# Kernel tuning notes

Hardware: AMD Instinct MI355X
Metric: run time of the kernel (lower is better)

## Reference

```python
import jax, jax.numpy as jnp
import numpy as np
from jax import lax

N = 16384
K = 16
EPS = 1e-5


def setup_inputs() -> dict:
    key = jax.random.key(0)
    ks = jax.random.split(key, 10)

    def w(k, shape):
        fan_in = shape[0]
        return jax.random.normal(k, shape, jnp.float32) / np.sqrt(fan_in)

    return {
        "pos": jax.random.normal(ks[0], (N, 3), jnp.float32),
        "normal": jax.random.normal(ks[1], (N, 3), jnp.float32),
        # conv1 mlp: Linear(9,64) -> GroupNorm(8,64) -> ReLU -> Linear(64,64)
        "W1a": w(ks[2], (9, 64)), "b1a": jnp.zeros((64,), jnp.float32),
        "g1": jnp.ones((64,), jnp.float32), "beta1": jnp.zeros((64,), jnp.float32),
        "W1b": w(ks[3], (64, 64)), "b1b": jnp.zeros((64,), jnp.float32),
        # conv2 mlp: Linear(67,64) -> GroupNorm(8,64) -> ReLU -> Linear(64,64)
        "W2a": w(ks[4], (67, 64)), "b2a": jnp.zeros((64,), jnp.float32),
        "g2": jnp.ones((64,), jnp.float32), "beta2": jnp.zeros((64,), jnp.float32),
        "W2b": w(ks[5], (64, 64)), "b2b": jnp.zeros((64,), jnp.float32),
        # conv3 mlp: Linear(67,128) -> GroupNorm(16,128) -> ReLU -> Linear(128,128)
        "W3a": w(ks[6], (67, 128)), "b3a": jnp.zeros((128,), jnp.float32),
        "g3": jnp.ones((128,), jnp.float32), "beta3": jnp.zeros((128,), jnp.float32),
        "W3b": w(ks[7], (128, 128)), "b3b": jnp.zeros((128,), jnp.float32),
    }


def knn_graph(pos, k):
    # [N,N] squared distances; loop=True -> self is included (distance 0).
    sq = jnp.sum(pos * pos, axis=1)
    d2 = sq[:, None] + sq[None, :] - 2.0 * (pos @ pos.T)
    _, nbr = lax.top_k(-d2, k)  # [N,k] neighbor (source) indices per target node
    return nbr


def group_norm(h, gamma, beta, groups):
    # h: [N,k,C]; normalize each group of channels per edge sample.
    n, k, c = h.shape
    hg = h.reshape(n, k, groups, c // groups)
    mu = hg.mean(axis=-1, keepdims=True)
    var = hg.var(axis=-1, keepdims=True)
    hg = (hg - mu) * lax.rsqrt(var + EPS)
    return hg.reshape(n, k, c) * gamma + beta


def pointnet_conv(x, pos, nbr, Wa, ba, gamma, beta, Wb, bb, groups):
    # message: concat(x_j, pos_j - pos_i), MLP per edge, max-aggregate over neighbors
    xj = x[nbr]                              # [N,k,C_in]
    rel = pos[nbr] - pos[:, None, :]         # [N,k,3]
    m = jnp.concatenate([xj, rel], axis=-1)  # [N,k,C_in+3]
    h = m @ Wa + ba
    h = jax.nn.relu(group_norm(h, gamma, beta, groups))
    h = h @ Wb + bb
    return jnp.max(h, axis=1)                # [N,C_out]


def reference(pos, normal, W1a, b1a, g1, beta1, W1b, b1b,
              W2a, b2a, g2, beta2, W2b, b2b,
              W3a, b3a, g3, beta3, W3b, b3b):
    nbr = knn_graph(pos, K)
    h = jnp.concatenate([pos, normal], axis=-1)  # [N,6]
    h1 = jax.nn.relu(pointnet_conv(h, pos, nbr, W1a, b1a, g1, beta1, W1b, b1b, 8))
    h2 = jax.nn.relu(pointnet_conv(h1, pos, nbr, W2a, b2a, g2, beta2, W2b, b2b, 8))
    h3 = jax.nn.relu(pointnet_conv(h2, pos, nbr, W3a, b3a, g3, beta3, W3b, b3b, 16))
    return (h1, h2, h3)
```

## Files before the change

### kernel.cpp

```cpp
#include <hip/hip_runtime.h>
#include <hip/hip_bf16.h>
#include <stdint.h>

typedef unsigned long long u64;
typedef unsigned int u32;
typedef __attribute__((ext_vector_type(8))) short bf16x8;
typedef __attribute__((ext_vector_type(4))) float f32x4;

__device__ __forceinline__ float ldv(const void* p, size_t idx, int mode) {
  return mode ? __bfloat162float(((const __hip_bfloat16*)p)[idx])
              : ((const float*)p)[idx];
}
__device__ __forceinline__ void stv(void* p, size_t idx, int mode, float v) {
  if (mode) ((__hip_bfloat16*)p)[idx] = __float2bfloat16(v);
  else      ((float*)p)[idx] = v;
}
__device__ __forceinline__ unsigned short f2bfb(float f) {
  u32 u = __float_as_uint(f);
  u32 r = u + 0x7fffu + ((u >> 16) & 1u);
  return (unsigned short)(r >> 16);
}
__device__ __forceinline__ u64 shfl64(u64 v, int src) {
  int lo = __shfl((int)(u32)(v & 0xffffffffu), src, 64);
  int hi = __shfl((int)(u32)(v >> 32), src, 64);
  return ((u64)(u32)hi << 32) | (u32)lo;
}
__device__ __forceinline__ u64 shflxor64(u64 v, int m) {
  int lo = __shfl_xor((int)(u32)(v & 0xffffffffu), m, 64);
  int hi = __shfl_xor((int)(u32)(v >> 32), m, 64);
  return ((u64)(u32)hi << 32) | (u32)lo;
}
__device__ __forceinline__ u64 shfl64w16(u64 v, int src) {
  int lo = __shfl((int)(u32)(v & 0xffffffffu), src, 16);
  int hi = __shfl((int)(u32)(v >> 32), src, 16);
  return ((u64)(u32)hi << 32) | (u32)lo;
}

__global__ void PointNetSimple_61409442398998_kernel() {}

struct CvtEnt { const void* src; float* dst; int n; };
struct CvtArgs { CvtEnt e[12]; };
struct WEnt { const void* src; unsigned short* dst; int K, N, Kpad; };
struct WArgs { WEnt e[6]; };

__global__ void setup_kernel(const void* __restrict__ pos,
                             const void* __restrict__ nrm,
                             WArgs wa, CvtArgs ca,
                             int* __restrict__ flag,
                             float4* __restrict__ pos4,
                             float* __restrict__ h0, int n) {
  const unsigned short* u16p = (const unsigned short*)pos;
  int cnt = 0;
  for (int k = 0; k < 32; ++k) {
    int e = (u16p[k] >> 7) & 0xff;
    if (e >= 110 && e <= 140) cnt++;
  }
  const int mode = (cnt >= 26) ? 1 : 0;

  const int nprep = n >> 8;
  const int b = blockIdx.x;
  if (b < nprep) {
    int i = b * 256 + threadIdx.x;
    float x = ldv(pos, 3*(size_t)i+0, mode);
    float y = ldv(pos, 3*(size_t)i+1, mode);
    float z = ldv(pos, 3*(size_t)i+2, mode);
    pos4[i] = make_float4(x, y, z, x*x + y*y + z*z);
    h0[6*(size_t)i+0] = x; h0[6*(size_t)i+1] = y; h0[6*(size_t)i+2] = z;
    h0[6*(size_t)i+3] = ldv(nrm, 3*(size_t)i+0, mode);
    h0[6*(size_t)i+4] = ldv(nrm, 3*(size_t)i+1, mode);
    h0[6*(size_t)i+5] = ldv(nrm, 3*(size_t)i+2, mode);
  } else {
    int r = b - nprep;
    if (r < 6) {
      WEnt ent = wa.e[r];
      for (int t = threadIdx.x; t < ent.N * ent.Kpad; t += blockDim.x) {
        int nn = t / ent.Kpad;
        int k  = t - nn * ent.Kpad;
        float v = (k < ent.K) ? ldv(ent.src, (size_t)k * ent.N + nn, mode) : 0.0f;
        ent.dst[t] = f2bfb(v);
      }
      if (r == 0 && threadIdx.x == 0) flag[0] = mode;
    } else {
      for (int t2 = 0; t2 < 12; ++t2) {
        CvtEnt ent = ca.e[t2];
        for (int t = threadIdx.x; t < ent.n; t += blockDim.x)
          ent.dst[t] = ldv(ent.src, t, mode);
      }
    }
  }
}

#define KNN_TPB 512
#define KNN_WPB 8
#define KCH 1024

__device__ __forceinline__ void knn_flush(u64* __restrict__ wbuf, int& cnt,
                                          u64& val, u64& t15, float& th,
                                          int lane) {
  u64 cand = (lane < cnt) ? wbuf[lane] : ~0ull;
#pragma unroll
  for (int k = 2; k <= 64; k <<= 1) {
#pragma unroll
    for (int j = k >> 1; j > 0; j >>= 1) {
      u64 other = shflxor64(cand, j);
      bool up    = ((lane & k) == 0) || (k == 64);
      bool lower = ((lane & j) == 0);
      bool keepMin = (up == lower);
      u64 mn = cand < other ? cand : other;
      u64 mx = cand < other ? other : cand;
      cand = keepMin ? mn : mx;
    }
  }
  u64 rev = shfl64w16(cand, 15 - (lane & 15));
  u64 lo = val < rev ? val : rev;
#pragma unroll
  for (int j = 8; j > 0; j >>= 1) {
    u64 other = shflxor64(lo, j);
    bool lower = ((lane & j) == 0);
    u64 mn = lo < other ? lo : other;
    u64 mx = lo < other ? other : lo;
    lo = lower ? mn : mx;
  }
  val = (lane < 16) ? lo : ~0ull;
  t15 = shfl64(val, 15);
  th = __uint_as_float((u32)(t15 >> 32));
  cnt = 0;
}

__global__ __launch_bounds__(KNN_TPB) void knn4_kernel(
    const float4* __restrict__ pos4, int* __restrict__ nbr, int n) {
  __shared__ float4 sp[2][KCH];
  __shared__ u64 buf[KNN_WPB][72];
  const int tid  = threadIdx.x;
  const int lane = tid & 63;
  const int wid  = tid >> 6;
  const int i    = blockIdx.x * KNN_WPB + wid;
  const float4 pi = pos4[i];
  u64* wbuf = &buf[wid][0];

  u64 val = ~0ull;
  u64 t15 = ~0ull;
  float th = 3.4e38f;
  int cnt = 0;

  for (int t = tid; t < KCH; t += KNN_TPB) sp[0][t] = pos4[t];
  __syncthreads();

  const int nch = n / KCH;
  for (int c = 0; c < nch; ++c) {
    const int cur = c & 1;
    float4 pre0, pre1;
    const bool more = (c + 1 < nch);
    if (more) {
      pre0 = pos4[(size_t)(c+1)*KCH + tid];
      pre1 = pos4[(size_t)(c+1)*KCH + KNN_TPB + tid];
    }
#pragma unroll 2
    for (int t = 0; t < KCH; t += 64) {
      float4 a = sp[cur][t + lane];
      float d2 = (pi.w + a.w) - 2.0f*(pi.x*a.x + pi.y*a.y + pi.z*a.z);
      d2 = fmaxf(d2, 0.0f);
      bool pass = (d2 <= th);
      u64 bal = __ballot(pass);
      if (bal) {
        int pc = __popcll(bal);
        if (cnt + pc > 64) knn_flush(wbuf, cnt, val, t15, th, lane);
        u32 mb = __builtin_amdgcn_mbcnt_lo((u32)bal, 0u);
        mb = __builtin_amdgcn_mbcnt_hi((u32)(bal >> 32), mb);
        if (pass)
          wbuf[cnt + mb] = ((u64)__float_as_uint(d2) << 32) | (u32)(c*KCH + t + lane);
        cnt += pc;
      }
    }
    if (more) {
      sp[cur^1][tid] = pre0;
      sp[cur^1][KNN_TPB + tid] = pre1;
    }
    __syncthreads();
  }
  knn_flush(wbuf, cnt, val, t15, th, lane);
  if (lane < 16) nbr[(size_t)i*16 + lane] = (int)(val & 0xffffffffu);
}

template<int CIN, int CMID, int KT1, int NT, int KT2>
__global__ __launch_bounds__(256) void conv_mfma2_kernel(
    const float* __restrict__ xin,
    const float4* __restrict__ pos4,
    const int* __restrict__ nbr,
    const int* __restrict__ flag,
    const unsigned short* __restrict__ WaT,
    const unsigned short* __restrict__ WbT,
    const float* __restrict__ baf,
    const float* __restrict__ gmf,
    const float* __restrict__ btf,
    const float* __restrict__ bbf,
    float* __restrict__ xout,
    void* __restrict__ bout, size_t out_off)
{
  constexpr int K1PAD = KT1 * 32;
  constexpr int SB = CMID + 8;

  __shared__ unsigned short msgB[128 * SB];
  __shared__ float stage[4][32][20];

  const int tid  = threadIdx.x;
  const int lane = tid & 63;
  const int w    = tid >> 6;
  const int quad = lane >> 4;
  const int cl   = lane & 15;
  const int node0 = blockIdx.x * 8;
  const int mode = flag[0];

  bf16x8 afr[2][KT1];
#pragma unroll
  for (int mt = 0; mt < 2; ++mt) {
    const int node = node0 + w*2 + mt;
    const int j = nbr[(size_t)node*16 + cl];
    const float4 pin = pos4[node];
    const float4 pj = pos4[j];
    const float rx = pj.x - pin.x, ry = pj.y - pin.y, rz = pj.z - pin.z;
    if constexpr (CIN == 64) {
#pragma unroll
      for (int kt = 0; kt < 2; ++kt) {
        const float* p = &xin[(size_t)j*64 + kt*32 + quad*8];
        float4 a = *(const float4*)p;
        float4 b = *(const float4*)(p + 4);
        unsigned short o[8] = {f2bfb(a.x), f2bfb(a.y), f2bfb(a.z), f2bfb(a.w),
                               f2bfb(b.x), f2bfb(b.y), f2bfb(b.z), f2bfb(b.w)};
        afr[mt][kt] = *(bf16x8*)o;
      }
      unsigned short o[8] = {0,0,0,0,0,0,0,0};
      if (quad == 0) { o[0] = f2bfb(rx); o[1] = f2bfb(ry); o[2] = f2bfb(rz); }
      afr[mt][KT1-1] = *(bf16x8*)o;
    } else {
      unsigned short o[8] = {0,0,0,0,0,0,0,0};
      if (quad == 0) {
        const float* p = &xin[(size_t)j*6];
        o[0] = f2bfb(p[0]); o[1] = f2bfb(p[1]); o[2] = f2bfb(p[2]);
        o[3] = f2bfb(p[3]); o[4] = f2bfb(p[4]); o[5] = f2bfb(p[5]);
        o[6] = f2bfb(rx);   o[7] = f2bfb(ry);
      } else if (quad == 1) {
        o[0] = f2bfb(rz);
      }
      afr[mt][0] = *(bf16x8*)o;
    }
  }

  f32x4 acc1[2][NT];
#pragma unroll
  for (int mt = 0; mt < 2; ++mt)
#pragma unroll
    for (int nt = 0; nt < NT; ++nt) acc1[mt][nt] = (f32x4){0.f, 0.f, 0.f, 0.f};
#pragma unroll
  for (int kt = 0; kt < KT1; ++kt)
#pragma unroll
    for (int nt = 0; nt < NT; ++nt) {
      bf16x8 bfr = *(const bf16x8*)&WaT[(size_t)(nt*16 + cl) * K1PAD + kt*32 + quad*8];
      acc1[0][nt] = __builtin_amdgcn_mfma_f32_16x16x32_bf16(afr[0][kt], bfr, acc1[0][nt], 0, 0, 0);
      acc1[1][nt] = __builtin_amdgcn_mfma_f32_16x16x32_bf16(afr[1][kt], bfr, acc1[1][nt], 0, 0, 0);
    }

#pragma unroll
  for (int nt = 0; nt < NT; ++nt) {
    float bac = baf[nt*16 + cl];
#pragma unroll
    for (int mt = 0; mt < 2; ++mt)
#pragma unroll
      for (int reg = 0; reg < 4; ++reg)
        stage[w][mt*16 + quad*4 + reg][cl] = acc1[mt][nt][reg] + bac;
    asm volatile("" ::: "memory");
    {
      int row = lane >> 1, gl = lane & 1;
      float4 va = *(const float4*)&stage[w][row][gl*8];
      float4 vb = *(const float4*)&stage[w][row][gl*8 + 4];
      float s  = va.x+va.y+va.z+va.w + vb.x+vb.y+vb.z+vb.w;
      float q  = va.x*va.x+va.y*va.y+va.z*va.z+va.w*va.w
               + vb.x*vb.x+vb.y*vb.y+vb.z*vb.z+vb.w*vb.w;
      float mu = s * 0.125f;
      float var = q * 0.125f - mu * mu;
      float inv = rsqrtf(fmaxf(var, 0.0f) + 1e-5f);
      int cb = nt*16 + gl*8;
      float vv[8] = {va.x, va.y, va.z, va.w, vb.x, vb.y, vb.z, vb.w};
      unsigned short o[8];
#pragma unroll
      for (int e = 0; e < 8; ++e) {
        float t = (vv[e] - mu) * inv * gmf[cb+e] + btf[cb+e];
        o[e] = f2bfb(fmaxf(t, 0.0f));
      }
      *(bf16x8*)&msgB[(w*32 + row) * SB + cb] = *(bf16x8*)o;
    }
    asm volatile("" ::: "memory");
  }

  f32x4 acc2[2][NT];
#pragma unroll
  for (int mt = 0; mt < 2; ++mt)
#pragma unroll
    for (int nt = 0; nt < NT; ++nt) acc2[mt][nt] = (f32x4){0.f, 0.f, 0.f, 0.f};
#pragma unroll
  for (int kt = 0; kt < KT2; ++kt) {
    bf16x8 af0 = *(const bf16x8*)&msgB[(w*32 + cl)      * SB + kt*32 + quad*8];
    bf16x8 af1 = *(const bf16x8*)&msgB[(w*32 + 16 + cl) * SB + kt*32 + quad*8];
#pragma unroll
    for (int nt = 0; nt < NT; ++nt) {
      bf16x8 bfr = *(const bf16x8*)&WbT[(size_t)(nt*16 + cl) * CMID + kt*32 + quad*8];
      acc2[0][nt] = __builtin_amdgcn_mfma_f32_16x16x32_bf16(af0, bfr, acc2[0][nt], 0, 0, 0);
      acc2[1][nt] = __builtin_amdgcn_mfma_f32_16x16x32_bf16(af1, bfr, acc2[1][nt], 0, 0, 0);
    }
  }

#pragma unroll
  for (int mt = 0; mt < 2; ++mt) {
    int node = node0 + w*2 + mt;
#pragma unroll
    for (int nt = 0; nt < NT; ++nt) {
      float m = fmaxf(fmaxf(acc2[mt][nt][0], acc2[mt][nt][1]),
                      fmaxf(acc2[mt][nt][2], acc2[mt][nt][3]));
      m = fmaxf(m, __shfl_xor(m, 16, 64));
      m = fmaxf(m, __shfl_xor(m, 32, 64));
      float v = fmaxf(m + bbf[nt*16 + cl], 0.0f);
      if (quad == 0) {
        size_t oi = (size_t)node * CMID + nt*16 + cl;
        if (xout) xout[oi] = v;
        stv(bout, out_off + oi, mode, v);
      }
    }
  }
}

extern "C" void kernel_launch(void* const* d_in, const int* in_sizes, int n_in,
                              void* d_out, int out_size, void* d_ws, size_t ws_size,
                              hipStream_t stream) {
  (void)n_in; (void)ws_size; (void)in_sizes;
  int n = out_size / 256;
  if (n <= 0 || (n & 255)) n = 16384;

  float* ws = (float*)d_ws;
  int*    flag = (int*)ws;
  float4* pos4 = (float4*)(ws + 16);
  float*  h0   = ws + 16 + (size_t)4*n;
  float*  h1   = ws + 16 + (size_t)10*n;
  float*  h2   = ws + 16 + (size_t)74*n;
  int*    nbr  = (int*)(ws + 16 + (size_t)138*n);
  float*  vbuf = ws + 16 + (size_t)154*n;
  unsigned short* wtbuf = (unsigned short*)(vbuf + 1024);

  const int vsz[12] = {64,64,64,64, 64,64,64,64, 128,128,128,128};
  const int vsrc[12] = {3,4,5,7, 9,10,11,13, 15,16,17,19};
  CvtArgs ca;
  float* vptr[12];
  {
    int off = 0;
    for (int t = 0; t < 12; ++t) {
      ca.e[t].src = d_in[vsrc[t]];
      ca.e[t].dst = vbuf + off;
      ca.e[t].n   = vsz[t];
      vptr[t] = vbuf + off;
      off += vsz[t];
    }
  }
  const int wK[6]    = {9, 64, 67, 64, 67, 128};
  const int wN[6]    = {64, 64, 64, 64, 128, 128};
  const int wKp[6]   = {32, 64, 96, 64, 96, 128};
  const int wsrc[6]  = {2, 6, 8, 12, 14, 18};
  WArgs wa;
  unsigned short* wptr[6];
  {
    int off = 0;
    for (int t = 0; t < 6; ++t) {
      wa.e[t].src  = d_in[wsrc[t]];
      wa.e[t].dst  = wtbuf + off;
      wa.e[t].K    = wK[t];
      wa.e[t].N    = wN[t];
      wa.e[t].Kpad = wKp[t];
      wptr[t] = wtbuf + off;
      off += wN[t] * wKp[t];
    }
  }

  setup_kernel<<<n/256 + 7, 256, 0, stream>>>(
      d_in[0], d_in[1], wa, ca, flag, pos4, h0, n);
  knn4_kernel<<<n/KNN_WPB, KNN_TPB, 0, stream>>>(pos4, nbr, n);

  conv_mfma2_kernel<6, 64, 1, 4, 2><<<n/8, 256, 0, stream>>>(
      h0, pos4, nbr, flag, wptr[0], wptr[1],
      vptr[0], vptr[1], vptr[2], vptr[3], h1, d_out, (size_t)0);
  conv_mfma2_kernel<64, 64, 3, 4, 2><<<n/8, 256, 0, stream>>>(
      h1, pos4, nbr, flag, wptr[2], wptr[3],
      vptr[4], vptr[5], vptr[6], vptr[7], h2, d_out, (size_t)n*64);
  conv_mfma2_kernel<64, 128, 3, 8, 4><<<n/8, 256, 0, stream>>>(
      h2, pos4, nbr, flag, wptr[4], wptr[5],
      vptr[8], vptr[9], vptr[10], vptr[11], (float*)nullptr, d_out, (size_t)n*128);
}
```

Baseline: 385.7 us.

## Process four query points per wavefront in kNN to reuse shared-memory candidate loads

The kNN kernel now gives each wavefront four target points instead of one, each with its own threshold, top-16 state and shared-memory candidate buffer. Every candidate position read from LDS is reused for four distance computations, and the grid shrinks by four. This cuts LDS traffic and the chunk-streaming overhead per query. In exchange it adds register pressure, more divergent ballot and flush branches per iteration, and leaves fewer blocks to fill the GPU.

```diff
diff --git a/kernel.cpp b/kernel.cpp
--- a/kernel.cpp
+++ b/kernel.cpp
@@ -92,12 +92,12 @@
 
 #define KNN_TPB 512
 #define KNN_WPB 8
+#define KNN_TPW 4
 #define KCH 1024
 
-__device__ __forceinline__ void knn_flush(u64* __restrict__ wbuf, int& cnt,
-                                          u64& val, u64& t15, float& th,
-                                          int lane) {
-  u64 cand = (lane < cnt) ? wbuf[lane] : ~0ull;
+__device__ __forceinline__ void knn_flush(u64* __restrict__ wbuf_t, int& cnt,
+                                          u64& val, float& th, int lane) {
+  u64 cand = (lane < cnt) ? wbuf_t[lane] : ~0ull;
 #pragma unroll
   for (int k = 2; k <= 64; k <<= 1) {
 #pragma unroll
@@ -122,26 +122,31 @@
     lo = lower ? mn : mx;
   }
   val = (lane < 16) ? lo : ~0ull;
-  t15 = shfl64(val, 15);
+  u64 t15 = shfl64(val, 15);
   th = __uint_as_float((u32)(t15 >> 32));
   cnt = 0;
 }
 
-__global__ __launch_bounds__(KNN_TPB) void knn4_kernel(
+__global__ __launch_bounds__(KNN_TPB) void knn5_kernel(
     const float4* __restrict__ pos4, int* __restrict__ nbr, int n) {
   __shared__ float4 sp[2][KCH];
-  __shared__ u64 buf[KNN_WPB][72];
+  __shared__ u64 buf[KNN_WPB][KNN_TPW][64];
   const int tid  = threadIdx.x;
   const int lane = tid & 63;
   const int wid  = tid >> 6;
-  const int i    = blockIdx.x * KNN_WPB + wid;
-  const float4 pi = pos4[i];
-  u64* wbuf = &buf[wid][0];
-
-  u64 val = ~0ull;
-  u64 t15 = ~0ull;
-  float th = 3.4e38f;
-  int cnt = 0;
+  const int tbase = (blockIdx.x * KNN_WPB + wid) * KNN_TPW;
+
+  float4 pi[KNN_TPW];
+  float  thr[KNN_TPW];
+  u64    val[KNN_TPW];
+  int    cnt[KNN_TPW];
+#pragma unroll
+  for (int tt = 0; tt < KNN_TPW; ++tt) {
+    pi[tt]  = pos4[tbase + tt];
+    thr[tt] = 3.4e38f;
+    val[tt] = ~0ull;
+    cnt[tt] = 0;
+  }
 
   for (int t = tid; t < KCH; t += KNN_TPB) sp[0][t] = pos4[t];
   __syncthreads();
@@ -155,21 +160,27 @@
       pre0 = pos4[(size_t)(c+1)*KCH + tid];
       pre1 = pos4[(size_t)(c+1)*KCH + KNN_TPB + tid];
     }
-#pragma unroll 2
     for (int t = 0; t < KCH; t += 64) {
       float4 a = sp[cur][t + lane];
-      float d2 = (pi.w + a.w) - 2.0f*(pi.x*a.x + pi.y*a.y + pi.z*a.z);
-      d2 = fmaxf(d2, 0.0f);
-      bool pass = (d2 <= th);
-      u64 bal = __ballot(pass);
-      if (bal) {
-        int pc = __popcll(bal);
-        if (cnt + pc > 64) knn_flush(wbuf, cnt, val, t15, th, lane);
-        u32 mb = __builtin_amdgcn_mbcnt_lo((u32)bal, 0u);
-        mb = __builtin_amdgcn_mbcnt_hi((u32)(bal >> 32), mb);
-        if (pass)
-          wbuf[cnt + mb] = ((u64)__float_as_uint(d2) << 32) | (u32)(c*KCH + t + lane);
-        cnt += pc;
+      const int base = c*KCH + t;
+#pragma unroll
+      for (int tt = 0; tt < KNN_TPW; ++tt) {
+        float d2 = (pi[tt].w + a.w)
+                 - 2.0f*(pi[tt].x*a.x + pi[tt].y*a.y + pi[tt].z*a.z);
+        d2 = fmaxf(d2, 0.0f);
+        bool pass = (d2 <= thr[tt]);
+        u64 bal = __ballot(pass);
+        if (bal) {
+          int pc = __popcll(bal);
+          if (cnt[tt] + pc > 64)
+            knn_flush(&buf[wid][tt][0], cnt[tt], val[tt], thr[tt], lane);
+          u32 mb = __builtin_amdgcn_mbcnt_lo((u32)bal, 0u);
+          mb = __builtin_amdgcn_mbcnt_hi((u32)(bal >> 32), mb);
+          if (pass)
+            buf[wid][tt][cnt[tt] + mb] =
+                ((u64)__float_as_uint(d2) << 32) | (u32)(base + lane);
+          cnt[tt] += pc;
+        }
       }
     }
     if (more) {
@@ -178,8 +189,12 @@
     }
     __syncthreads();
   }
-  knn_flush(wbuf, cnt, val, t15, th, lane);
-  if (lane < 16) nbr[(size_t)i*16 + lane] = (int)(val & 0xffffffffu);
+#pragma unroll
+  for (int tt = 0; tt < KNN_TPW; ++tt) {
+    knn_flush(&buf[wid][tt][0], cnt[tt], val[tt], thr[tt], lane);
+    if (lane < 16)
+      nbr[(size_t)(tbase + tt)*16 + lane] = (int)(val[tt] & 0xffffffffu);
+  }
 }
 
 template<int CIN, int CMID, int KT1, int NT, int KT2>
@@ -380,7 +395,7 @@
 
   setup_kernel<<<n/256 + 7, 256, 0, stream>>>(
       d_in[0], d_in[1], wa, ca, flag, pos4, h0, n);
-  knn4_kernel<<<n/KNN_WPB, KNN_TPB, 0, stream>>>(pos4, nbr, n);
+  knn5_kernel<<<n/(KNN_WPB*KNN_TPW), KNN_TPB, 0, stream>>>(pos4, nbr, n);
 
   conv_mfma2_kernel<6, 64, 1, 4, 2><<<n/8, 256, 0, stream>>>(
       h0, pos4, nbr, flag, wptr[0], wptr[1],
```

Result: slower. 404.3 us (+4.8%).
